# Kernel optimization log

Measured on AMD Instinct MI355X. Metric: run time of the kernel, lower is better.

Reference implementation:

```python
import jax, jax.numpy as jnp
import numpy as np

IMG_H, IMG_W = 1024, 1024
STRIDES = (8, 16, 32, 64, 128)
NUM_CLASSES = 80
CONF_THR = 0.05
IOU_THR = 0.5
MAX_PER_CLASS = 100
MAX_DET = 100
K_CAND = 256  # candidates kept per class before greedy NMS (pre-sort cap)


def build_grids():
    gy, gx, gs = [], [], []
    for s in STRIDES:
        H, W = IMG_H // s, IMG_W // s
        h = jnp.arange(H, dtype=jnp.float32)
        w = jnp.arange(W, dtype=jnp.float32)
        gy_, gx_ = jnp.meshgrid(h, w)  # 'xy' indexing -> shape [W, H], matches tf.meshgrid
        gy.append(gy_.reshape(-1))
        gx.append(gx_.reshape(-1))
        gs.append(jnp.full((W * H,), float(s), dtype=jnp.float32))
    return jnp.concatenate(gy), jnp.concatenate(gx), jnp.concatenate(gs)


def pairwise_iou(b):
    # b: [K,4] as (y1, x1, y2, x2)
    y1, x1, y2, x2 = b[:, 0], b[:, 1], b[:, 2], b[:, 3]
    area = (y2 - y1) * (x2 - x1)
    ih = jnp.maximum(jnp.minimum(y2[:, None], y2[None, :]) - jnp.maximum(y1[:, None], y1[None, :]), 0.0)
    iw = jnp.maximum(jnp.minimum(x2[:, None], x2[None, :]) - jnp.maximum(x1[:, None], x1[None, :]), 0.0)
    inter = ih * iw
    union = area[:, None] + area[None, :] - inter
    return inter / jnp.maximum(union, 1e-8)


def nms_one_class(boxes, scores):
    # boxes [N,4], scores [N] -> (sel_boxes [MAX_PER_CLASS,4], sel_scores [MAX_PER_CLASS])
    top_s, idx = jax.lax.top_k(scores, K_CAND)
    cand = boxes[idx]                       # [K,4]
    valid = top_s > CONF_THR
    iou = jax.lax.stop_gradient(pairwise_iou(cand))  # suppression mask is non-differentiable
    rng = jnp.arange(K_CAND)

    def body(i, keep):
        sup = (iou[i] > IOU_THR) & (rng > i) & keep[i]
        return keep & ~sup

    keep = jax.lax.fori_loop(0, K_CAND, body, valid)
    kept = jnp.where(keep, top_s, 0.0)
    sel_s, sel_i = jax.lax.top_k(kept, MAX_PER_CLASS)
    return cand[sel_i], sel_s


def combined_nms(boxes, scores):
    # per image: boxes [N,4] shared across classes, scores [N,C]
    cls_boxes, cls_scores = jax.vmap(nms_one_class, in_axes=(None, 1))(boxes, scores)
    C = scores.shape[1]
    cls_labels = jnp.broadcast_to(jnp.arange(C, dtype=jnp.float32)[:, None], cls_scores.shape)
    flat_s = cls_scores.reshape(-1)
    flat_b = cls_boxes.reshape(-1, 4)
    flat_l = cls_labels.reshape(-1)
    fin_s, fin_i = jax.lax.top_k(flat_s, MAX_DET)
    fin_b = flat_b[fin_i] * (fin_s > 0.0)[:, None].astype(flat_b.dtype)  # zero pad boxes like TF
    fin_l = flat_l[fin_i]
    return fin_b, fin_l, fin_s


def decode(pred_regs, pred_ctrs, pred_clfs):
    gy, gx, gs = build_grids()
    gy, gx, gs = gy[:, None], gx[:, None], gs[:, None]     # [N,1]
    score = pred_clfs * pred_ctrs                           # [B,N,C]
    x1 = gx - pred_regs[..., 0:1]
    x2 = gx + pred_regs[..., 1:2]
    y1 = gy - pred_regs[..., 2:3]
    y2 = gy + pred_regs[..., 3:4]
    bbox = jnp.concatenate([y1, x1, y2, x2], axis=-1) * gs  # [B,N,4] in image coords
    return jax.vmap(combined_nms)(bbox, score)


def setup_inputs() -> dict:
    key = jax.random.key(0)
    k1, k2, k3 = jax.random.split(key, 3)
    N = sum((IMG_H // s) * (IMG_W // s) for s in STRIDES)  # 21824
    B = 16
    return {
        "pred_regs": jax.random.uniform(k1, (B, N, 4), jnp.float32),
        "pred_ctrs": jax.random.uniform(k2, (B, N, 1), jnp.float32),
        "pred_clfs": jax.random.uniform(k3, (B, N, NUM_CLASSES), jnp.float32),
    }


def reference(pred_regs, pred_ctrs, pred_clfs):
    # returns (final_bboxes [B,100,4], final_labels [B,100] float, final_scores [B,100])
    return decode(pred_regs, pred_ctrs, pred_clfs)
```

## Files before the change

### kernel.cpp

```cpp
#include <hip/hip_runtime.h>
#include <stdint.h>

#pragma clang fp contract(off)

namespace {
constexpr int kN = 21824;
constexpr int kB = 16;
constexpr int kC = 80;
constexpr int kK = 256;
constexpr int kMaxPC = 100;
constexpr int kMaxDet = 100;
constexpr int kBins1 = 2048;
constexpr int kCap = 1536;
constexpr int kSortN = 512;
constexpr int kRows = kB * kC;
constexpr int kTiles = kN / 64;
constexpr int kTPB = 6;
constexpr int kGScan = (kTiles + kTPB - 1) / kTPB;
constexpr int kLCap = 48;
constexpr float kThr = 0.72f;
}

__device__ __forceinline__ uint64_t make_key(float s, int n) {
  return ((uint64_t)__float_as_uint(s) << 16) | (uint32_t)(0xFFFF - n);
}

__device__ uint32_t block_scan_incl(uint32_t val) {
  __shared__ uint32_t wsum[4];
  int lane = threadIdx.x & 63;
  int wave = threadIdx.x >> 6;
  for (int d = 1; d < 64; d <<= 1) {
    uint32_t t = __shfl_up(val, (unsigned)d, 64);
    if (lane >= d) val += t;
  }
  if (lane == 63) wsum[wave] = val;
  __syncthreads();
  uint32_t off = 0;
  for (int w = 0; w < wave; ++w) off += wsum[w];
  __syncthreads();
  return val + off;
}

struct RegSrc {
  uint64_t k[6];
  int cnt;
  template <class F> __device__ void each(F f) const {
    #pragma unroll
    for (int j = 0; j < 6; ++j)
      if (j < cnt) f(k[j]);
  }
};
struct ColSrc {
  const float* cl;
  const float* ct;
  template <class F> __device__ void each(F f) const {
    for (int n = threadIdx.x; n < kN; n += 256)
      f(make_key(cl[(size_t)n * kC] * ct[n], n));
  }
};
struct ArrSrc {
  const float* s;
  int count;
  template <class F> __device__ void each(F f) const {
    for (int i = threadIdx.x; i < count; i += 256) f(make_key(s[i], i));
  }
};

template <class Src, bool FAST>
__device__ int refine_gather(const Src& src, int K, int cap,
                             uint32_t* hist, uint64_t* cbuf) {
  __shared__ int sel_bin;
  __shared__ uint32_t sel_hd, sel_above, qcnt;
  int tid = threadIdx.x;

  for (int i = tid; i < kBins1; i += 256) hist[i] = 0;
  __syncthreads();
  src.each([&](uint64_t k) {
    uint32_t bin = FAST ? (uint32_t)((k >> 28) & 0x7FF) : (uint32_t)(k >> 37);
    atomicAdd(&hist[bin], 1u);
  });
  __syncthreads();
  uint32_t krem = (uint32_t)K;
  {
    uint32_t bl[8], v = 0;
    int base = kBins1 - 1 - 8 * tid;
    for (int j = 0; j < 8; ++j) { bl[j] = hist[base - j]; v += bl[j]; }
    uint32_t S = block_scan_incl(v);
    if (S >= krem && (S - v) < krem) {
      uint32_t cum = S - v;
      for (int j = 0; j < 8; ++j) {
        cum += bl[j];
        if (cum >= krem) { sel_bin = base - j; sel_hd = bl[j]; sel_above = cum - bl[j]; break; }
      }
    }
    __syncthreads();
  }
  uint64_t prefix = FAST ? (uint64_t)(0x3F000u | (uint32_t)sel_bin)
                         : (uint64_t)sel_bin;
  int shift = FAST ? 28 : 37;
  krem = (uint32_t)K - sel_above;
  uint32_t Sge = ((uint32_t)K - krem) + sel_hd;
  __syncthreads();

  while (Sge > (uint32_t)cap) {
    int w = (shift > 8) ? 8 : shift;
    int ns = shift - w, bins = 1 << w, hs = shift;
    for (int i = tid; i < bins; i += 256) hist[i] = 0;
    __syncthreads();
    uint64_t pfx = prefix;
    src.each([&](uint64_t k) {
      if ((k >> hs) == pfx)
        atomicAdd(&hist[(uint32_t)(k >> ns) & (bins - 1)], 1u);
    });
    __syncthreads();
    uint32_t v = (tid < bins) ? hist[bins - 1 - tid] : 0;
    uint32_t S = block_scan_incl(v);
    if (v && S >= krem && (S - v) < krem) {
      sel_bin = bins - 1 - tid; sel_hd = v; sel_above = S - v;
    }
    __syncthreads();
    prefix = (prefix << w) | (uint32_t)sel_bin;
    krem -= sel_above;
    Sge = ((uint32_t)K - krem) + sel_hd;
    shift = ns;
    __syncthreads();
  }

  uint64_t L = prefix << shift;
  if (tid == 0) qcnt = 0;
  __syncthreads();
  src.each([&](uint64_t k) {
    if (k >= L) {
      uint32_t p = atomicAdd(&qcnt, 1u);
      if (p < (uint32_t)cap) cbuf[p] = k;
    }
  });
  __syncthreads();
  int Scnt = (int)qcnt;
  return Scnt > cap ? cap : Scnt;
}

__device__ __forceinline__ void bitonic512_desc(uint64_t* sortb) {
  int tid = threadIdx.x;
  uint64_t e0 = sortb[2 * tid], e1 = sortb[2 * tid + 1];
  #pragma unroll
  for (int k2 = 2; k2 <= kSortN; k2 <<= 1) {
    #pragma unroll
    for (int j = k2 >> 1; j >= 2; j >>= 1) {
      bool up = ((tid & (k2 >> 1)) == 0);
      uint64_t p0, p1;
      bool low;
      if (j >= 128) {
        __syncthreads();
        sortb[2 * tid] = e0; sortb[2 * tid + 1] = e1;
        __syncthreads();
        int pi = (2 * tid) ^ j;
        p0 = sortb[pi]; p1 = sortb[pi + 1];
        low = ((tid & (j >> 1)) == 0);
      } else {
        int d = j >> 1;
        p0 = (uint64_t)__shfl_xor((unsigned long long)e0, d, 64);
        p1 = (uint64_t)__shfl_xor((unsigned long long)e1, d, 64);
        low = ((tid & d) == 0);
      }
      bool keepMax = (up == low);
      e0 = (keepMax == (e0 > p0)) ? e0 : p0;
      e1 = (keepMax == (e1 > p1)) ? e1 : p1;
    }
    {
      bool up = ((tid & (k2 >> 1)) == 0);
      bool sw = up ? (e0 < e1) : (e0 > e1);
      uint64_t t0 = sw ? e1 : e0, t1 = sw ? e0 : e1;
      e0 = t0; e1 = t1;
    }
  }
  __syncthreads();
  sortb[2 * tid] = e0; sortb[2 * tid + 1] = e1;
  __syncthreads();
}

__global__ __launch_bounds__(256) void score_scan_kernel(
    const float* __restrict__ clfs, const float* __restrict__ ctrs,
    uint32_t* __restrict__ gcnt, uint64_t* __restrict__ glist) {
  int b = blockIdx.y;
  int t0 = blockIdx.x * kTPB;
  int t1 = t0 + kTPB; if (t1 > kTiles) t1 = kTiles;
  int nbase = t0 * 64;
  int nanch = (t1 - t0) * 64;

  __shared__ uint64_t lbuf[kC][kLCap + 1];
  __shared__ uint32_t lcnt[kC];
  __shared__ uint32_t gbase[kC];
  __shared__ float ct[kTPB * 64];
  int tid = threadIdx.x;
  for (int i = tid; i < kC; i += 256) lcnt[i] = 0;
  for (int i = tid; i < nanch; i += 256) ct[i] = ctrs[(size_t)b * kN + nbase + i];
  __syncthreads();

  const float4* src = (const float4*)(clfs + ((size_t)b * kN + nbase) * kC);
  int n4 = nanch * (kC / 4);
  float4 v = (tid < n4) ? src[tid] : float4{0, 0, 0, 0};
  for (int e = tid; e < n4; e += 256) {
    int en = e + 256;
    float4 vn = (en < n4) ? src[en] : float4{0, 0, 0, 0};
    int a = e / 20;
    int c0 = (e % 20) * 4;
    float cv = ct[a];
    int n = nbase + a;
    float sv[4] = {v.x * cv, v.y * cv, v.z * cv, v.w * cv};
    #pragma unroll
    for (int j = 0; j < 4; ++j) {
      if (sv[j] > kThr) {
        int c = c0 + j;
        uint32_t p = atomicAdd(&lcnt[c], 1u);
        if (p < kLCap) lbuf[c][p] = make_key(sv[j], n);
      }
    }
    v = vn;
  }
  __syncthreads();

  if (tid < kC) {
    uint32_t m = lcnt[tid];
    int row = b * kC + tid;
    if (m > kLCap) {
      atomicAdd(&gcnt[row], (uint32_t)(kCap + 1));
      gbase[tid] = 0xFFFFFFFFu;
    } else {
      gbase[tid] = m ? atomicAdd(&gcnt[row], m) : 0u;
    }
  }
  __syncthreads();

  int lane = tid & 63, wave = tid >> 6;
  for (int c = wave * 20; c < wave * 20 + 20; ++c) {
    uint32_t m = lcnt[c];
    uint32_t base = gbase[c];
    if (base == 0xFFFFFFFFu || m == 0) continue;
    if (m > kLCap) m = kLCap;
    int row = b * kC + c;
    for (uint32_t i = lane; i < m; i += 64) {
      uint32_t p = base + i;
      if (p < kCap) glist[(size_t)row * kCap + p] = lbuf[c][i];
    }
  }
}

__device__ __forceinline__ uint32_t iou_word32(
    const float4& A, float aA, const float4* boxes, const float* areas,
    uint32_t mask) {
  uint32_t cur = 0;
  #pragma unroll 8
  for (int s = 31; s >= 0; --s) {
    const float4 Bx = boxes[s];
    float aB = areas[s];
    float yy1 = fmaxf(A.x, Bx.x);
    float yy2 = fminf(A.z, Bx.z);
    float xx1 = fmaxf(A.y, Bx.y);
    float xx2 = fminf(A.w, Bx.w);
    float ih = fmaxf(yy2 - yy1, 0.0f);
    float iw = fmaxf(xx2 - xx1, 0.0f);
    float inter = ih * iw;
    float un = (aB + aA) - inter;
    float unc = fmaxf(un, 1e-8f);
    cur = (cur << 1) | (uint32_t)(inter + inter > unc);
  }
  return cur & mask;
}

__device__ __forceinline__ void iou_row_words(
    const float4& A, float aA, const float4* boxes, const float* areas,
    uint32_t (*sup)[8], int row, int lo, int hi ) {
  int w0 = lo >> 5, w1 = (hi - 1) >> 5;
  uint32_t mb = 0xFFFFFFFFu << (lo & 31);
  uint32_t me = (hi & 31) ? ((1u << (hi & 31)) - 1u) : 0xFFFFFFFFu;
  for (int w = w0; w <= w1; ++w) {
    uint32_t mask = 0xFFFFFFFFu;
    if (w == w0) mask &= mb;
    if (w == w1) mask &= me;
    uint32_t cur = iou_word32(A, aA, boxes + (w << 5), areas + (w << 5), mask);
    if (cur) atomicOr(&sup[row][w], cur);
  }
}

__global__ __launch_bounds__(256, 5) void nms_class_kernel(
    const uint32_t* __restrict__ gcnt, const uint64_t* __restrict__ glist,
    const float* __restrict__ clfs, const float* __restrict__ ctrs,
    const float* __restrict__ regs,
    float* __restrict__ cls_boxes, float* __restrict__ cls_scores) {
  int row = blockIdx.x;
  int b = row / kC, c = row % kC;
  int tid = threadIdx.x;
  int lane = tid & 63, wave = tid >> 6;

  __shared__ union alignas(16) {
    uint32_t hist[kBins1];
    uint64_t sortb[kSortN];
    uint32_t supm[kK][8];
  } hu;
  __shared__ float4 boxf4[kK];
  __shared__ float barea[kK];
  __shared__ uint64_t kinit[4];
  __shared__ uint64_t kfin[4];

  uint32_t cnt = gcnt[row];
  int Scnt;
  if (cnt >= (uint32_t)kK && cnt <= (uint32_t)kCap) {
    RegSrc rs; rs.cnt = 0;
    const uint64_t* gl = glist + (size_t)row * kCap;
    #pragma unroll
    for (int j = 0; j < 6; ++j) {
      int i = tid + j * 256;
      if (i < (int)cnt) { rs.k[j] = gl[i]; rs.cnt = j + 1; }
    }
    Scnt = refine_gather<RegSrc, true>(rs, kK, kSortN, hu.hist, hu.sortb);
  } else {
    ColSrc cs{clfs + (size_t)b * kN * kC + c, ctrs + (size_t)b * kN};
    Scnt = refine_gather<ColSrc, false>(cs, kK, kSortN, hu.hist, hu.sortb);
  }

  for (int i = Scnt + tid; i < kSortN; i += 256) hu.sortb[i] = 0;
  __syncthreads();
  bitonic512_desc(hu.sortb);
  uint64_t myk = hu.sortb[tid];
  __syncthreads();

  int n = 0xFFFF - (int)(myk & 0xFFFF);
  float sc_v = __uint_as_float((uint32_t)(myk >> 16));
  int off, hl;
  float sf;
  if (n < 16384)      { off = 0;     hl = 7; sf = 8.f;   }
  else if (n < 20480) { off = 16384; hl = 6; sf = 16.f;  }
  else if (n < 21504) { off = 20480; hl = 5; sf = 32.f;  }
  else if (n < 21760) { off = 21504; hl = 4; sf = 64.f;  }
  else                { off = 21760; hl = 3; sf = 128.f; }
  int kk = n - off;
  float gx = (float)(kk >> hl);
  float gy = (float)(kk & ((1 << hl) - 1));
  const float4 r = ((const float4*)regs)[(size_t)b * kN + n];
  float4 mybox;
  mybox.x = (gy - r.z) * sf;
  mybox.y = (gx - r.x) * sf;
  mybox.z = (gy + r.w) * sf;
  mybox.w = (gx + r.y) * sf;
  float my_a = (mybox.z - mybox.x) * (mybox.w - mybox.y);
  boxf4[tid] = mybox;
  barea[tid] = my_a;
  unsigned long long vm = __ballot(sc_v > 0.05f);
  if (lane == 0) kinit[wave] = vm;
  {
    uint64_t* sp = (uint64_t*)&hu.supm[0][0];
    #pragma unroll
    for (int q = 0; q < 4; ++q) sp[tid + q * 256] = 0;
  }
  __syncthreads();

  if (tid < 128) {
    iou_row_words(mybox, my_a, boxf4, barea, hu.supm, tid, tid + 1, tid + 128);
  } else {
    int T = tid - 128;
    float4 bA = boxf4[T]; float aA = barea[T];
    iou_row_words(bA, aA, boxf4, barea, hu.supm, T, T + 128, 256);
    if (T > 0) {
      int rB = 255 - T;
      float4 bB = boxf4[rB]; float aB = barea[rB];
      iou_row_words(bB, aB, boxf4, barea, hu.supm, rB, 256 - T, 256);
    }
  }
  __syncthreads();

  if (wave == 0) {
    uint64_t kw0 = kinit[0], kw1 = kinit[1], kw2 = kinit[2], kw3 = kinit[3];
    #define NMS_SECTION(W, KW)                                              \
      _Pragma("unroll")                                                     \
      for (int ch = 0; ch < 16; ++ch) {                                     \
        const ulonglong2* s0 = (const ulonglong2*)hu.supm[(W << 6) + ch * 4 + 0]; \
        const ulonglong2* s1 = (const ulonglong2*)hu.supm[(W << 6) + ch * 4 + 1]; \
        const ulonglong2* s2 = (const ulonglong2*)hu.supm[(W << 6) + ch * 4 + 2]; \
        const ulonglong2* s3 = (const ulonglong2*)hu.supm[(W << 6) + ch * 4 + 3]; \
        ulonglong2 aL = s0[0], aH = s0[1];                                  \
        ulonglong2 bL = s1[0], bH = s1[1];                                  \
        ulonglong2 cL = s2[0], cH = s2[1];                                  \
        ulonglong2 dL = s3[0], dH = s3[1];                                  \
        if ((KW >> (ch * 4 + 0)) & 1ull) { kw0 &= ~aL.x; kw1 &= ~aL.y; kw2 &= ~aH.x; kw3 &= ~aH.y; } \
        if ((KW >> (ch * 4 + 1)) & 1ull) { kw0 &= ~bL.x; kw1 &= ~bL.y; kw2 &= ~bH.x; kw3 &= ~bH.y; } \
        if ((KW >> (ch * 4 + 2)) & 1ull) { kw0 &= ~cL.x; kw1 &= ~cL.y; kw2 &= ~cH.x; kw3 &= ~cH.y; } \
        if ((KW >> (ch * 4 + 3)) & 1ull) { kw0 &= ~dL.x; kw1 &= ~dL.y; kw2 &= ~dH.x; kw3 &= ~dH.y; } \
      }
    NMS_SECTION(0, kw0)
    NMS_SECTION(1, kw1)
    NMS_SECTION(2, kw2)
    NMS_SECTION(3, kw3)
    #undef NMS_SECTION
    if (lane == 0) { kfin[0] = kw0; kfin[1] = kw1; kfin[2] = kw2; kfin[3] = kw3; }
  }
  __syncthreads();

  uint64_t kw0 = kfin[0], kw1 = kfin[1], kw2 = kfin[2], kw3 = kfin[3];
  uint64_t ww = (wave == 0) ? kw0 : (wave == 1) ? kw1 : (wave == 2) ? kw2 : kw3;
  bool keptf = (ww >> lane) & 1ull;
  int kept_total = (int)(__popcll(kw0) + __popcll(kw1) +
                         __popcll(kw2) + __popcll(kw3));
  int kept_before = (int)__popcll(ww & ((1ull << lane) - 1ull));
  if (wave > 0) kept_before += (int)__popcll(kw0);
  if (wave > 1) kept_before += (int)__popcll(kw1);
  if (wave > 2) kept_before += (int)__popcll(kw2);

  int rank2 = keptf ? kept_before : (kept_total + tid - kept_before);
  if (rank2 < kMaxPC) {
    float ks = keptf ? sc_v : 0.0f;
    size_t obase = ((size_t)row) * kMaxPC + rank2;
    cls_scores[obase] = ks;
    float* ob = cls_boxes + obase * 4;
    ob[0] = mybox.x; ob[1] = mybox.y; ob[2] = mybox.z; ob[3] = mybox.w;
  }
}

__global__ __launch_bounds__(256) void final_topk_kernel(
    const float* __restrict__ cls_scores, const float* __restrict__ cls_boxes,
    float* __restrict__ out) {
  int b = blockIdx.x;
  int tid = threadIdx.x;
  const int M = kC * kMaxPC;
  __shared__ union alignas(16) {
    uint32_t hist[kBins1];
    uint64_t sortb[kSortN];
  } hu;

  ArrSrc as{cls_scores + (size_t)b * M, M};
  int Scnt = refine_gather<ArrSrc, false>(as, kMaxDet, kSortN, hu.hist, hu.sortb);

  for (int i = Scnt + tid; i < kSortN; i += 256) hu.sortb[i] = 0;
  __syncthreads();
  bitonic512_desc(hu.sortb);

  if (tid < kMaxDet) {
    uint64_t myk = hu.sortb[tid];
    float sv = __uint_as_float((uint32_t)(myk >> 16));
    int f = 0xFFFF - (int)(myk & 0xFFFF);
    int cls = f / 100;
    const float* bp = cls_boxes + ((size_t)b * M + f) * 4;
    float m = (sv > 0.0f) ? 1.0f : 0.0f;
    float* ob = out + ((size_t)b * kMaxDet + tid) * 4;
    ob[0] = bp[0] * m; ob[1] = bp[1] * m; ob[2] = bp[2] * m; ob[3] = bp[3] * m;
    out[(size_t)kB * kMaxDet * 4 + (size_t)b * kMaxDet + tid] = (float)cls;
    out[(size_t)kB * kMaxDet * 5 + (size_t)b * kMaxDet + tid] = sv;
  }
}

extern "C" void kernel_launch(void* const* d_in, const int* in_sizes, int n_in,
                              void* d_out, int out_size, void* d_ws, size_t ws_size,
                              hipStream_t stream) {
  (void)in_sizes; (void)n_in; (void)out_size;
  const float* regs = (const float*)d_in[0];
  const float* ctrs = (const float*)d_in[1];
  const float* clfs = (const float*)d_in[2];
  float* out = (float*)d_out;

  const size_t glB  = (size_t)kRows * kCap * sizeof(uint64_t);
  const size_t cbB  = (size_t)kRows * kMaxPC * 4 * sizeof(float);
  const size_t csB  = (size_t)kRows * kMaxPC * sizeof(float);
  const size_t cntB = 8192;
  if (ws_size < glB + cbB + csB + cntB) return;

  char* p = (char*)d_ws;
  uint64_t* glist   = (uint64_t*)p; p += glB;
  float* cls_boxes  = (float*)p;    p += cbB;
  float* cls_scores = (float*)p;    p += csB;
  uint32_t* gcnt    = (uint32_t*)p;

  hipMemsetAsync(gcnt, 0, (size_t)kRows * sizeof(uint32_t), stream);
  score_scan_kernel<<<dim3(kGScan, kB), 256, 0, stream>>>(clfs, ctrs, gcnt, glist);
  nms_class_kernel<<<kRows, 256, 0, stream>>>(gcnt, glist, clfs, ctrs, regs,
                                              cls_boxes, cls_scores);
  final_topk_kernel<<<kB, 256, 0, stream>>>(cls_scores, cls_boxes, out);
}
```

Baseline: 269.3 us.

## Use wave-aggregated atomics for candidate gather and restructure IoU mask computation

```diff
diff --git a/kernel.cpp b/kernel.cpp
--- a/kernel.cpp
+++ b/kernel.cpp
@@ -49,6 +49,10 @@
     for (int j = 0; j < 6; ++j)
       if (j < cnt) f(k[j]);
   }
+  template <class F> __device__ void each2(F f) const {
+    #pragma unroll
+    for (int j = 0; j < 6; ++j) f(k[j], j < cnt);
+  }
 };
 struct ColSrc {
   const float* cl;
@@ -57,12 +61,28 @@
     for (int n = threadIdx.x; n < kN; n += 256)
       f(make_key(cl[(size_t)n * kC] * ct[n], n));
   }
+  template <class F> __device__ void each2(F f) const {
+    constexpr int kNr = (kN + 255) & ~255;
+    for (int n = threadIdx.x; n < kNr; n += 256) {
+      bool v = n < kN;
+      float s = v ? cl[(size_t)n * kC] * ct[n] : 0.0f;
+      f(make_key(s, n), v);
+    }
+  }
 };
 struct ArrSrc {
   const float* s;
   int count;
   template <class F> __device__ void each(F f) const {
     for (int i = threadIdx.x; i < count; i += 256) f(make_key(s[i], i));
+  }
+  template <class F> __device__ void each2(F f) const {
+    int cr = (count + 255) & ~255;
+    for (int i = threadIdx.x; i < cr; i += 256) {
+      bool v = i < count;
+      float sv = v ? s[i] : 0.0f;
+      f(make_key(sv, i), v);
+    }
   }
 };
 
@@ -129,12 +149,21 @@
   uint64_t L = prefix << shift;
   if (tid == 0) qcnt = 0;
   __syncthreads();
-  src.each([&](uint64_t k) {
-    if (k >= L) {
-      uint32_t p = atomicAdd(&qcnt, 1u);
-      if (p < (uint32_t)cap) cbuf[p] = k;
-    }
-  });
+  {
+    int lane = tid & 63;
+    uint64_t lmask = (1ull << lane) - 1ull;
+    src.each2([&](uint64_t k, bool valid) {
+      bool q = valid && (k >= L);
+      unsigned long long m = __ballot(q);
+      uint32_t base = 0;
+      if (lane == 0 && m) base = atomicAdd(&qcnt, (uint32_t)__popcll(m));
+      base = __shfl(base, 0, 64);
+      if (q) {
+        uint32_t p = base + (uint32_t)__popcll(m & lmask);
+        if (p < (uint32_t)cap) cbuf[p] = k;
+      }
+    });
+  }
   __syncthreads();
   int Scnt = (int)qcnt;
   return Scnt > cap ? cap : Scnt;
@@ -246,44 +275,7 @@
   }
 }
 
-__device__ __forceinline__ uint32_t iou_word32(
-    const float4& A, float aA, const float4* boxes, const float* areas,
-    uint32_t mask) {
-  uint32_t cur = 0;
-  #pragma unroll 8
-  for (int s = 31; s >= 0; --s) {
-    const float4 Bx = boxes[s];
-    float aB = areas[s];
-    float yy1 = fmaxf(A.x, Bx.x);
-    float yy2 = fminf(A.z, Bx.z);
-    float xx1 = fmaxf(A.y, Bx.y);
-    float xx2 = fminf(A.w, Bx.w);
-    float ih = fmaxf(yy2 - yy1, 0.0f);
-    float iw = fmaxf(xx2 - xx1, 0.0f);
-    float inter = ih * iw;
-    float un = (aB + aA) - inter;
-    float unc = fmaxf(un, 1e-8f);
-    cur = (cur << 1) | (uint32_t)(inter + inter > unc);
-  }
-  return cur & mask;
-}
-
-__device__ __forceinline__ void iou_row_words(
-    const float4& A, float aA, const float4* boxes, const float* areas,
-    uint32_t (*sup)[8], int row, int lo, int hi ) {
-  int w0 = lo >> 5, w1 = (hi - 1) >> 5;
-  uint32_t mb = 0xFFFFFFFFu << (lo & 31);
-  uint32_t me = (hi & 31) ? ((1u << (hi & 31)) - 1u) : 0xFFFFFFFFu;
-  for (int w = w0; w <= w1; ++w) {
-    uint32_t mask = 0xFFFFFFFFu;
-    if (w == w0) mask &= mb;
-    if (w == w1) mask &= me;
-    uint32_t cur = iou_word32(A, aA, boxes + (w << 5), areas + (w << 5), mask);
-    if (cur) atomicOr(&sup[row][w], cur);
-  }
-}
-
-__global__ __launch_bounds__(256, 5) void nms_class_kernel(
+__global__ __launch_bounds__(256) void nms_class_kernel(
     const uint32_t* __restrict__ gcnt, const uint64_t* __restrict__ glist,
     const float* __restrict__ clfs, const float* __restrict__ ctrs,
     const float* __restrict__ regs,
@@ -355,16 +347,30 @@
   }
   __syncthreads();
 
-  if (tid < 128) {
-    iou_row_words(mybox, my_a, boxf4, barea, hu.supm, tid, tid + 1, tid + 128);
-  } else {
-    int T = tid - 128;
-    float4 bA = boxf4[T]; float aA = barea[T];
-    iou_row_words(bA, aA, boxf4, barea, hu.supm, T, T + 128, 256);
-    if (T > 0) {
-      int rB = 255 - T;
-      float4 bB = boxf4[rB]; float aB = barea[rB];
-      iou_row_words(bB, aB, boxf4, barea, hu.supm, rB, 256 - T, 256);
+  {
+    int tw = tid >> 5;
+    uint32_t meq = 0xFFFFFFFEu << (tid & 31);
+    for (int w = wave << 1; w < 8; ++w) {
+      const float4* bp = boxf4 + (w << 5);
+      const float* ap = barea + (w << 5);
+      uint32_t cur = 0;
+      #pragma unroll
+      for (int s = 0; s < 32; ++s) {
+        const float4 Bx = bp[s];
+        float aB = ap[s];
+        float yy1 = fmaxf(mybox.x, Bx.x);
+        float yy2 = fminf(mybox.z, Bx.z);
+        float xx1 = fmaxf(mybox.y, Bx.y);
+        float xx2 = fminf(mybox.w, Bx.w);
+        float ih = fmaxf(yy2 - yy1, 0.0f);
+        float iw = fmaxf(xx2 - xx1, 0.0f);
+        float inter = ih * iw;
+        float un = (aB + my_a) - inter;
+        float unc = fmaxf(un, 1e-8f);
+        cur |= (inter + inter > unc) ? (1u << s) : 0u;
+      }
+      uint32_t mask = (w > tw) ? 0xFFFFFFFFu : ((w == tw) ? meq : 0u);
+      if (mask) hu.supm[tid][w] = cur & mask;
     }
   }
   __syncthreads();
```

Measured after the change: 270.5 us. Within noise of the previous version (+0.4%).
